# Optimization experiments

Hardware: AMD Instinct MI355X
Metric: run time of the kernel (lower is better)

## Reference

```python
import jax, jax.numpy as jnp
import numpy as np

B, N, D_PAIR, D_HID = 1, 512, 128, 128

def _layernorm(x, gamma, beta, eps=1e-5):
    mu = jnp.mean(x, axis=-1, keepdims=True)
    var = jnp.mean(jnp.square(x - mu), axis=-1, keepdims=True)
    return (x - mu) * jax.lax.rsqrt(var + eps) * gamma + beta

def setup_inputs() -> dict:
    key = jax.random.key(0)
    ks = jax.random.split(key, 8)
    s = 0.02  # small init scale for weights
    return {
        "z": jax.random.normal(ks[0], (B, N, N, D_PAIR), dtype=jnp.float32),
        "mask": jnp.ones((B, N, N), dtype=jnp.float32),
        "w_ab_p": jax.random.normal(ks[1], (2 * D_HID, D_PAIR), dtype=jnp.float32) * s,
        "b_ab_p": jnp.zeros((2 * D_HID,), dtype=jnp.float32),
        "w_ab_g": jax.random.normal(ks[2], (2 * D_HID, D_PAIR), dtype=jnp.float32) * s,
        "b_ab_g": jnp.zeros((2 * D_HID,), dtype=jnp.float32),
        "w_g": jax.random.normal(ks[3], (D_PAIR, D_PAIR), dtype=jnp.float32) * s,
        "b_g": jnp.zeros((D_PAIR,), dtype=jnp.float32),
        "w_z": jax.random.normal(ks[4], (D_PAIR, D_HID), dtype=jnp.float32) * s,
        "b_z": jnp.zeros((D_PAIR,), dtype=jnp.float32),
        "ln_in_g": jnp.ones((D_PAIR,), dtype=jnp.float32),
        "ln_in_b": jnp.zeros((D_PAIR,), dtype=jnp.float32),
        "ln_out_g": jnp.ones((D_HID,), dtype=jnp.float32),
        "ln_out_b": jnp.zeros((D_HID,), dtype=jnp.float32),
    }

def reference(z, mask, w_ab_p, b_ab_p, w_ab_g, b_ab_g, w_g, b_g, w_z, b_z,
              ln_in_g, ln_in_b, ln_out_g, ln_out_b):
    z_ = _layernorm(z, ln_in_g, ln_in_b)                      # [B,N,N,c_z]
    ab = (z_ @ w_ab_p.T + b_ab_p) * jax.nn.sigmoid(z_ @ w_ab_g.T + b_ab_g)
    ab = ab * mask[..., None]                                 # [B,N,N,2h]
    a, b = jnp.split(ab, 2, axis=-1)                          # [B,N,N,h] each
    # outgoing=True: sum over k of a[i,k,d]*b[j,k,d]
    x = jnp.einsum('bikd,bjkd->bijd', a, b)                   # [B,N,N,h]
    g = jax.nn.sigmoid(z @ w_g.T + b_g)                       # [B,N,N,c_z]
    out = g * (_layernorm(x, ln_out_g, ln_out_b) @ w_z.T + b_z)
    return out
```

## Files before the change

### kernel.cpp

```cpp
#include <hip/hip_runtime.h>
#include <stdint.h>

#define NSEQ 512
#define DPAIR 128
#define NN (NSEQ*NSEQ)
#define LDPAD 136

typedef unsigned short u16;
typedef __attribute__((ext_vector_type(8))) short bf16x8;
typedef __attribute__((ext_vector_type(4))) float f32x4;

__device__ __forceinline__ float bf2f(u16 h){ return __uint_as_float(((uint32_t)h)<<16); }
__device__ __forceinline__ u16 f2bf(float f){
  uint32_t u = __float_as_uint(f);
  u += 0x7fffu + ((u>>16)&1u);
  return (u16)(u>>16);
}
__device__ __forceinline__ uint32_t cvtpk(float lo, float hi){
  uint32_t r;
  asm("v_cvt_pk_bf16_f32 %0, %1, %2" : "=v"(r) : "v"(lo), "v"(hi));
  return r;
}
__device__ __forceinline__ float sigmoidf_(float x){ return 1.0f/(1.0f+__expf(-x)); }

__device__ __forceinline__ void stage_w64(const float* __restrict__ src, u16* wb, int t){
  const float4* ws = (const float4*)src;
  #pragma unroll
  for (int i=0;i<8;i++){
    int e4 = i*256 + t; int r = e4>>5, c4 = e4&31;
    float4 v = ws[e4];
    uint2 pk;
    pk.x = cvtpk(v.x, v.y);
    pk.y = cvtpk(v.z, v.w);
    *(uint2*)&wb[r*LDPAD + c4*4] = pk;
  }
}

__device__ __forceinline__ void gemm_64x64(const u16* A, const u16* W,
                                           int wm, int wn, int fr, int fq,
                                           f32x4 (&acc)[2][2]){
  #pragma unroll
  for (int kk=0;kk<4;kk++){
    bf16x8 aF[2], bF[2];
    #pragma unroll
    for (int mi=0;mi<2;mi++) aF[mi] = *(const bf16x8*)(A + (wm+mi*16+fr)*LDPAD + kk*32 + fq*8);
    #pragma unroll
    for (int ni=0;ni<2;ni++) bF[ni] = *(const bf16x8*)(W + (wn+ni*16+fr)*LDPAD + kk*32 + fq*8);
    #pragma unroll
    for (int mi=0;mi<2;mi++)
      #pragma unroll
      for (int ni=0;ni<2;ni++)
        acc[mi][ni] = __builtin_amdgcn_mfma_f32_16x16x32_bf16(aF[mi], bF[ni], acc[mi][ni], 0, 0, 0);
  }
}

__global__ __launch_bounds__(256) void k1_proj(
    const float* __restrict__ z, const float* __restrict__ mask,
    const float* __restrict__ w_ab_p, const float* __restrict__ b_ab_p,
    const float* __restrict__ w_ab_g, const float* __restrict__ b_ab_g,
    const float* __restrict__ w_g, const float* __restrict__ b_g,
    const float* __restrict__ ln_g, const float* __restrict__ ln_b,
    u16* __restrict__ a_t, u16* __restrict__ b_t, u16* __restrict__ g_out)
{
  __shared__ u16 zr[64*LDPAD];
  __shared__ u16 zn[64*LDPAD];
  __shared__ u16 wb[64*LDPAD];
  __shared__ float lng[DPAIR], lnb[DPAIR], msk[64];

  const int t = threadIdx.x;
  const int p0 = blockIdx.x * 64;
  const int lane = t & 63, wv = t >> 6;
  const int wm = (wv >> 1) * 32, wn = (wv & 1) * 32;
  const int fr = lane & 15, fq = lane >> 4;

  if (t < DPAIR){ lng[t] = ln_g[t]; lnb[t] = ln_b[t]; }
  else if (t < DPAIR + 64) msk[t - DPAIR] = mask[p0 + t - DPAIR];

  {
    const float4* zs = (const float4*)(z + (size_t)p0 * DPAIR);
    #pragma unroll
    for (int i=0;i<8;i++){
      int e4 = i*256 + t; int pos = e4>>5, c4 = e4&31;
      float4 v = zs[e4];
      uint2 pk;
      pk.x = cvtpk(v.x, v.y);
      pk.y = cvtpk(v.z, v.w);
      *(uint2*)&zr[pos*LDPAD + c4*4] = pk;
    }
  }
  __syncthreads();
  {
    int pos = t>>2, q = t&3;
    float s=0.f, s2=0.f;
    #pragma unroll
    for (int j=0;j<32;j++){ float v = bf2f(zr[pos*LDPAD + q*32 + j]); s += v; s2 += v*v; }
    s  += __shfl_xor(s, 1);  s2 += __shfl_xor(s2, 1);
    s  += __shfl_xor(s, 2);  s2 += __shfl_xor(s2, 2);
    float mu  = s * (1.f/128.f);
    float var = s2 * (1.f/128.f) - mu*mu;
    float rs  = rsqrtf(var + 1e-5f);
    #pragma unroll
    for (int j=0;j<32;j++){
      int c = q*32 + j;
      float v = bf2f(zr[pos*LDPAD + c]);
      zn[pos*LDPAD + c] = f2bf((v - mu)*rs*lng[c] + lnb[c]);
    }
  }

  for (int nt=0; nt<4; nt++){
    __syncthreads();
    stage_w64(w_ab_p + nt*64*DPAIR, wb, t);
    __syncthreads();
    f32x4 accP[2][2] = {};
    gemm_64x64(zn, wb, wm, wn, fr, fq, accP);
    __syncthreads();
    stage_w64(w_ab_g + nt*64*DPAIR, wb, t);
    __syncthreads();
    f32x4 accG[2][2] = {};
    gemm_64x64(zn, wb, wm, wn, fr, fq, accG);
    __syncthreads();
    #pragma unroll
    for (int mi=0;mi<2;mi++)
      #pragma unroll
      for (int ni=0;ni<2;ni++)
        #pragma unroll
        for (int r=0;r<4;r++){
          int pos = wm + mi*16 + fq*4 + r;
          int nl  = wn + ni*16 + fr;
          int ng  = nt*64 + nl;
          float p  = accP[mi][ni][r] + b_ab_p[ng];
          float gg = accG[mi][ni][r] + b_ab_g[ng];
          wb[nl*72 + pos] = f2bf(p * sigmoidf_(gg) * msk[pos]);
        }
    __syncthreads();
    u16* dst = (nt < 2) ? a_t : b_t;
    int dbase = (nt & 1) * 64;
    #pragma unroll
    for (int i=0;i<2;i++){
      int e8 = i*256 + t; int dl = e8>>3, pc = e8&7;
      uint4 v = *(const uint4*)&wb[dl*72 + pc*8];
      *(uint4*)&dst[(size_t)(dbase+dl)*NN + p0 + pc*8] = v;
    }
  }

  for (int nt=0; nt<2; nt++){
    __syncthreads();
    stage_w64(w_g + nt*64*DPAIR, wb, t);
    __syncthreads();
    f32x4 acc[2][2] = {};
    gemm_64x64(zr, wb, wm, wn, fr, fq, acc);
    #pragma unroll
    for (int mi=0;mi<2;mi++)
      #pragma unroll
      for (int ni=0;ni<2;ni++)
        #pragma unroll
        for (int r=0;r<4;r++){
          int pos = wm + mi*16 + fq*4 + r;
          int ng  = nt*64 + wn + ni*16 + fr;
          g_out[(size_t)(p0+pos)*DPAIR + ng] = f2bf(sigmoidf_(acc[mi][ni][r] + b_g[ng]));
        }
  }
}

__global__ __launch_bounds__(256) void k2_einsum(
    const u16* __restrict__ a_t, const u16* __restrict__ b_t, u16* __restrict__ x_t)
{
  __shared__ u16 As[128*40];
  __shared__ u16 Bs[128*40];
  const int t = threadIdx.x;
  const int d  = blockIdx.z;
  const int i0 = blockIdx.x * 128;
  const int j0 = blockIdx.y * 128;
  const u16* Ag = a_t + (size_t)d*NN + (size_t)i0*NSEQ;
  const u16* Bg = b_t + (size_t)d*NN + (size_t)j0*NSEQ;

  const int lane = t & 63, wv = t >> 6;
  const int wm = (wv >> 1) * 64, wn = (wv & 1) * 64;
  const int fr = lane & 15, fq = lane >> 4;

  f32x4 acc[4][4] = {};

  for (int k0 = 0; k0 < NSEQ; k0 += 32){
    __syncthreads();
    #pragma unroll
    for (int i=0;i<2;i++){
      int e = i*256 + t; int r = e>>2, c8 = e&3;
      uint4 va = *(const uint4*)(Ag + (size_t)r*NSEQ + k0 + c8*8);
      *(uint4*)&As[r*40 + c8*8] = va;
      uint4 vb = *(const uint4*)(Bg + (size_t)r*NSEQ + k0 + c8*8);
      *(uint4*)&Bs[r*40 + c8*8] = vb;
    }
    __syncthreads();
    bf16x8 aF[4], bF[4];
    #pragma unroll
    for (int mi=0;mi<4;mi++) aF[mi] = *(const bf16x8*)&As[(wm + mi*16 + fr)*40 + fq*8];
    #pragma unroll
    for (int ni=0;ni<4;ni++) bF[ni] = *(const bf16x8*)&Bs[(wn + ni*16 + fr)*40 + fq*8];
    #pragma unroll
    for (int mi=0;mi<4;mi++)
      #pragma unroll
      for (int ni=0;ni<4;ni++)
        acc[mi][ni] = __builtin_amdgcn_mfma_f32_16x16x32_bf16(aF[mi], bF[ni], acc[mi][ni], 0, 0, 0);
  }
  u16* Xg = x_t + (size_t)d*NN;
  #pragma unroll
  for (int mi=0;mi<4;mi++)
    #pragma unroll
    for (int ni=0;ni<4;ni++)
      #pragma unroll
      for (int r=0;r<4;r++){
        int row = i0 + wm + mi*16 + fq*4 + r;
        int col = j0 + wn + ni*16 + fr;
        Xg[(size_t)row*NSEQ + col] = f2bf(acc[mi][ni][r]);
      }
}

__global__ __launch_bounds__(256) void k3_out(
    const u16* __restrict__ x_t, const u16* __restrict__ g_in,
    const float* __restrict__ w_z, const float* __restrict__ b_z,
    const float* __restrict__ ln_g, const float* __restrict__ ln_b,
    float* __restrict__ out)
{
  __shared__ u16 xs[64*LDPAD];
  __shared__ u16 wz[DPAIR*LDPAD];
  __shared__ float lng[DPAIR], lnb[DPAIR], bzs[DPAIR];

  const int t = threadIdx.x;
  const int p0 = blockIdx.x * 64;
  if (t < DPAIR){ lng[t] = ln_g[t]; lnb[t] = ln_b[t]; bzs[t] = b_z[t]; }

  {
    const float4* ws = (const float4*)w_z;
    #pragma unroll
    for (int i=0;i<16;i++){
      int e4 = i*256 + t; int r = e4>>5, c4 = e4&31;
      float4 v = ws[e4];
      uint2 pk;
      pk.x = cvtpk(v.x, v.y);
      pk.y = cvtpk(v.z, v.w);
      *(uint2*)&wz[r*LDPAD + c4*4] = pk;
    }
  }
  {
    #pragma unroll
    for (int i=0;i<8;i++){
      int e = i*256 + t; int dd = e>>4, pc = e&15;
      uint2 v = *(const uint2*)(x_t + (size_t)dd*NN + p0 + pc*4);
      int pb = pc*4;
      xs[(pb+0)*LDPAD + dd] = (u16)(v.x & 0xffffu);
      xs[(pb+1)*LDPAD + dd] = (u16)(v.x >> 16);
      xs[(pb+2)*LDPAD + dd] = (u16)(v.y & 0xffffu);
      xs[(pb+3)*LDPAD + dd] = (u16)(v.y >> 16);
    }
  }
  __syncthreads();
  {
    int pos = t>>2, q = t&3;
    float s=0.f, s2=0.f;
    #pragma unroll
    for (int j=0;j<32;j++){ float v = bf2f(xs[pos*LDPAD + q*32 + j]); s += v; s2 += v*v; }
    s  += __shfl_xor(s, 1);  s2 += __shfl_xor(s2, 1);
    s  += __shfl_xor(s, 2);  s2 += __shfl_xor(s2, 2);
    float mu  = s * (1.f/128.f);
    float var = s2 * (1.f/128.f) - mu*mu;
    float rs  = rsqrtf(var + 1e-5f);
    #pragma unroll
    for (int j=0;j<32;j++){
      int c = q*32 + j;
      float v = bf2f(xs[pos*LDPAD + c]);
      xs[pos*LDPAD + c] = f2bf((v - mu)*rs*lng[c] + lnb[c]);
    }
  }
  __syncthreads();
  const int lane = t & 63, wv = t >> 6;
  const int wm = (wv >> 1) * 32, wn = (wv & 1) * 64;
  const int fr = lane & 15, fq = lane >> 4;
  f32x4 acc[2][4] = {};
  #pragma unroll
  for (int kk=0;kk<4;kk++){
    bf16x8 aF[2], bF[4];
    #pragma unroll
    for (int mi=0;mi<2;mi++) aF[mi] = *(const bf16x8*)&xs[(wm+mi*16+fr)*LDPAD + kk*32 + fq*8];
    #pragma unroll
    for (int ni=0;ni<4;ni++) bF[ni] = *(const bf16x8*)&wz[(wn+ni*16+fr)*LDPAD + kk*32 + fq*8];
    #pragma unroll
    for (int mi=0;mi<2;mi++)
      #pragma unroll
      for (int ni=0;ni<4;ni++)
        acc[mi][ni] = __builtin_amdgcn_mfma_f32_16x16x32_bf16(aF[mi], bF[ni], acc[mi][ni], 0, 0, 0);
  }
  #pragma unroll
  for (int mi=0;mi<2;mi++)
    #pragma unroll
    for (int ni=0;ni<4;ni++)
      #pragma unroll
      for (int r=0;r<4;r++){
        int pos = wm + mi*16 + fq*4 + r;
        int c   = wn + ni*16 + fr;
        float gv = bf2f(g_in[(size_t)(p0+pos)*DPAIR + c]);
        out[(size_t)(p0+pos)*DPAIR + c] = gv * (acc[mi][ni][r] + bzs[c]);
      }
}

extern "C" void kernel_launch(void* const* d_in, const int* in_sizes, int n_in,
                              void* d_out, int out_size, void* d_ws, size_t ws_size,
                              hipStream_t stream)
{
  const float* z        = (const float*)d_in[0];
  const float* mask     = (const float*)d_in[1];
  const float* w_ab_p   = (const float*)d_in[2];
  const float* b_ab_p   = (const float*)d_in[3];
  const float* w_ab_g   = (const float*)d_in[4];
  const float* b_ab_g   = (const float*)d_in[5];
  const float* w_g      = (const float*)d_in[6];
  const float* b_g      = (const float*)d_in[7];
  const float* w_z      = (const float*)d_in[8];
  const float* b_z      = (const float*)d_in[9];
  const float* ln_in_g  = (const float*)d_in[10];
  const float* ln_in_b  = (const float*)d_in[11];
  const float* ln_out_g = (const float*)d_in[12];
  const float* ln_out_b = (const float*)d_in[13];
  float* out = (float*)d_out;

  const size_t plane = (size_t)DPAIR * NN;
  if (ws_size < 4 * plane * sizeof(u16)) return;

  u16* a_t = (u16*)d_ws;
  u16* b_t = a_t + plane;
  u16* g_b = b_t + plane;
  u16* x_t = g_b + plane;

  k1_proj<<<dim3(NN/64), dim3(256), 0, stream>>>(
      z, mask, w_ab_p, b_ab_p, w_ab_g, b_ab_g, w_g, b_g, ln_in_g, ln_in_b, a_t, b_t, g_b);
  k2_einsum<<<dim3(4, 4, DPAIR), dim3(256), 0, stream>>>(a_t, b_t, x_t);
  k3_out<<<dim3(NN/64), dim3(256), 0, stream>>>(x_t, g_b, w_z, b_z, ln_out_g, ln_out_b, out);
}
```

Measured before the change: 568.9 us.

## Restructure projection kernel: fused P/G staging, in-place layernorm, direct stores

The projection kernel now computes the output gate GEMM first with the full 128-row w_g staged at once, then layernorms z in place, freeing the separate normalized buffer. Each of the four ab tiles stages the P and G weight halves together into a doubled buffer and runs both GEMMs in one loop, cutting barriers per tile from six to about one. Transposed a/b results go straight from registers to global memory as 4-element packed stores instead of through a shared-memory transpose. The cost is narrower global stores (8 bytes each, spread across strided rows) in place of 16-byte coalesced ones, and a different shared-memory footprint.

```diff
diff --git a/kernel.cpp b/kernel.cpp
--- a/kernel.cpp
+++ b/kernel.cpp
@@ -22,37 +22,6 @@
   return r;
 }
 __device__ __forceinline__ float sigmoidf_(float x){ return 1.0f/(1.0f+__expf(-x)); }
-
-__device__ __forceinline__ void stage_w64(const float* __restrict__ src, u16* wb, int t){
-  const float4* ws = (const float4*)src;
-  #pragma unroll
-  for (int i=0;i<8;i++){
-    int e4 = i*256 + t; int r = e4>>5, c4 = e4&31;
-    float4 v = ws[e4];
-    uint2 pk;
-    pk.x = cvtpk(v.x, v.y);
-    pk.y = cvtpk(v.z, v.w);
-    *(uint2*)&wb[r*LDPAD + c4*4] = pk;
-  }
-}
-
-__device__ __forceinline__ void gemm_64x64(const u16* A, const u16* W,
-                                           int wm, int wn, int fr, int fq,
-                                           f32x4 (&acc)[2][2]){
-  #pragma unroll
-  for (int kk=0;kk<4;kk++){
-    bf16x8 aF[2], bF[2];
-    #pragma unroll
-    for (int mi=0;mi<2;mi++) aF[mi] = *(const bf16x8*)(A + (wm+mi*16+fr)*LDPAD + kk*32 + fq*8);
-    #pragma unroll
-    for (int ni=0;ni<2;ni++) bF[ni] = *(const bf16x8*)(W + (wn+ni*16+fr)*LDPAD + kk*32 + fq*8);
-    #pragma unroll
-    for (int mi=0;mi<2;mi++)
-      #pragma unroll
-      for (int ni=0;ni<2;ni++)
-        acc[mi][ni] = __builtin_amdgcn_mfma_f32_16x16x32_bf16(aF[mi], bF[ni], acc[mi][ni], 0, 0, 0);
-  }
-}
 
 __global__ __launch_bounds__(256) void k1_proj(
     const float* __restrict__ z, const float* __restrict__ mask,
@@ -63,14 +32,12 @@
     u16* __restrict__ a_t, u16* __restrict__ b_t, u16* __restrict__ g_out)
 {
   __shared__ u16 zr[64*LDPAD];
-  __shared__ u16 zn[64*LDPAD];
-  __shared__ u16 wb[64*LDPAD];
+  __shared__ u16 wb[128*LDPAD];
   __shared__ float lng[DPAIR], lnb[DPAIR], msk[64];
 
   const int t = threadIdx.x;
   const int p0 = blockIdx.x * 64;
   const int lane = t & 63, wv = t >> 6;
-  const int wm = (wv >> 1) * 32, wn = (wv & 1) * 32;
   const int fr = lane & 15, fq = lane >> 4;
 
   if (t < DPAIR){ lng[t] = ln_g[t]; lnb[t] = ln_b[t]; }
@@ -88,7 +55,51 @@
       *(uint2*)&zr[pos*LDPAD + c4*4] = pk;
     }
   }
-  __syncthreads();
+  {
+    const float4* ws = (const float4*)w_g;
+    #pragma unroll
+    for (int i=0;i<16;i++){
+      int e4 = i*256 + t; int r = e4>>5, c4 = e4&31;
+      float4 v = ws[e4];
+      uint2 pk;
+      pk.x = cvtpk(v.x, v.y);
+      pk.y = cvtpk(v.z, v.w);
+      *(uint2*)&wb[r*LDPAD + c4*4] = pk;
+    }
+  }
+  __syncthreads();
+
+  {
+    const int wm = (wv>>1)*32, wn2 = (wv&1)*64;
+    f32x4 acc[2][4] = {};
+    #pragma unroll
+    for (int kk=0;kk<4;kk++){
+      bf16x8 aF[2], bF[4];
+      #pragma unroll
+      for (int mi=0;mi<2;mi++) aF[mi] = *(const bf16x8*)&zr[(wm+mi*16+fr)*LDPAD + kk*32 + fq*8];
+      #pragma unroll
+      for (int ni=0;ni<4;ni++) bF[ni] = *(const bf16x8*)&wb[(wn2+ni*16+fr)*LDPAD + kk*32 + fq*8];
+      #pragma unroll
+      for (int mi=0;mi<2;mi++)
+        #pragma unroll
+        for (int ni=0;ni<4;ni++)
+          acc[mi][ni] = __builtin_amdgcn_mfma_f32_16x16x32_bf16(aF[mi], bF[ni], acc[mi][ni], 0, 0, 0);
+    }
+    #pragma unroll
+    for (int mi=0;mi<2;mi++)
+      #pragma unroll
+      for (int ni=0;ni<4;ni++){
+        int ng = wn2 + ni*16 + fr;
+        float bg = b_g[ng];
+        #pragma unroll
+        for (int r=0;r<4;r++){
+          int pos = wm + mi*16 + fq*4 + r;
+          g_out[(size_t)(p0+pos)*DPAIR + ng] = f2bf(sigmoidf_(acc[mi][ni][r] + bg));
+        }
+      }
+  }
+  __syncthreads();
+
   {
     int pos = t>>2, q = t&3;
     float s=0.f, s2=0.f;
@@ -103,62 +114,78 @@
     for (int j=0;j<32;j++){
       int c = q*32 + j;
       float v = bf2f(zr[pos*LDPAD + c]);
-      zn[pos*LDPAD + c] = f2bf((v - mu)*rs*lng[c] + lnb[c]);
-    }
-  }
-
+      zr[pos*LDPAD + c] = f2bf((v - mu)*rs*lng[c] + lnb[c]);
+    }
+  }
+  __syncthreads();
+
+  const int wm = (wv >> 1) * 32, wn = (wv & 1) * 32;
   for (int nt=0; nt<4; nt++){
+    {
+      const float4* wsP = (const float4*)(w_ab_p + (size_t)nt*64*DPAIR);
+      const float4* wsG = (const float4*)(w_ab_g + (size_t)nt*64*DPAIR);
+      #pragma unroll
+      for (int i=0;i<8;i++){
+        int e4 = i*256 + t; int r = e4>>5, c4 = e4&31;
+        float4 v = wsP[e4];
+        uint2 pk;
+        pk.x = cvtpk(v.x, v.y);
+        pk.y = cvtpk(v.z, v.w);
+        *(uint2*)&wb[r*LDPAD + c4*4] = pk;
+      }
+      #pragma unroll
+      for (int i=0;i<8;i++){
+        int e4 = i*256 + t; int r = e4>>5, c4 = e4&31;
+        float4 v = wsG[e4];
+        uint2 pk;
+        pk.x = cvtpk(v.x, v.y);
+        pk.y = cvtpk(v.z, v.w);
+        *(uint2*)&wb[(64+r)*LDPAD + c4*4] = pk;
+      }
+    }
     __syncthreads();
-    stage_w64(w_ab_p + nt*64*DPAIR, wb, t);
-    __syncthreads();
-    f32x4 accP[2][2] = {};
-    gemm_64x64(zn, wb, wm, wn, fr, fq, accP);
-    __syncthreads();
-    stage_w64(w_ab_g + nt*64*DPAIR, wb, t);
-    __syncthreads();
-    f32x4 accG[2][2] = {};
-    gemm_64x64(zn, wb, wm, wn, fr, fq, accG);
-    __syncthreads();
-    #pragma unroll
-    for (int mi=0;mi<2;mi++)
-      #pragma unroll
-      for (int ni=0;ni<2;ni++)
+    f32x4 accP[2][2] = {}, accG[2][2] = {};
+    #pragma unroll
+    for (int kk=0;kk<4;kk++){
+      bf16x8 aF[2], bP[2], bG[2];
+      #pragma unroll
+      for (int mi=0;mi<2;mi++) aF[mi] = *(const bf16x8*)&zr[(wm+mi*16+fr)*LDPAD + kk*32 + fq*8];
+      #pragma unroll
+      for (int ni=0;ni<2;ni++){
+        bP[ni] = *(const bf16x8*)&wb[(wn+ni*16+fr)*LDPAD + kk*32 + fq*8];
+        bG[ni] = *(const bf16x8*)&wb[(64+wn+ni*16+fr)*LDPAD + kk*32 + fq*8];
+      }
+      #pragma unroll
+      for (int mi=0;mi<2;mi++)
         #pragma unroll
-        for (int r=0;r<4;r++){
-          int pos = wm + mi*16 + fq*4 + r;
-          int nl  = wn + ni*16 + fr;
-          int ng  = nt*64 + nl;
-          float p  = accP[mi][ni][r] + b_ab_p[ng];
-          float gg = accG[mi][ni][r] + b_ab_g[ng];
-          wb[nl*72 + pos] = f2bf(p * sigmoidf_(gg) * msk[pos]);
+        for (int ni=0;ni<2;ni++){
+          accP[mi][ni] = __builtin_amdgcn_mfma_f32_16x16x32_bf16(aF[mi], bP[ni], accP[mi][ni], 0, 0, 0);
+          accG[mi][ni] = __builtin_amdgcn_mfma_f32_16x16x32_bf16(aF[mi], bG[ni], accG[mi][ni], 0, 0, 0);
         }
-    __syncthreads();
+    }
     u16* dst = (nt < 2) ? a_t : b_t;
     int dbase = (nt & 1) * 64;
     #pragma unroll
-    for (int i=0;i<2;i++){
-      int e8 = i*256 + t; int dl = e8>>3, pc = e8&7;
-      uint4 v = *(const uint4*)&wb[dl*72 + pc*8];
-      *(uint4*)&dst[(size_t)(dbase+dl)*NN + p0 + pc*8] = v;
-    }
-  }
-
-  for (int nt=0; nt<2; nt++){
+    for (int mi=0;mi<2;mi++){
+      int posb = wm + mi*16 + fq*4;
+      #pragma unroll
+      for (int ni=0;ni<2;ni++){
+        int nl   = wn + ni*16 + fr;
+        int ng   = nt*64 + nl;
+        int drow = dbase + nl;
+        float bp  = b_ab_p[ng];
+        float bgv = b_ab_g[ng];
+        float v0 = (accP[mi][ni][0]+bp) * sigmoidf_(accG[mi][ni][0]+bgv) * msk[posb+0];
+        float v1 = (accP[mi][ni][1]+bp) * sigmoidf_(accG[mi][ni][1]+bgv) * msk[posb+1];
+        float v2 = (accP[mi][ni][2]+bp) * sigmoidf_(accG[mi][ni][2]+bgv) * msk[posb+2];
+        float v3 = (accP[mi][ni][3]+bp) * sigmoidf_(accG[mi][ni][3]+bgv) * msk[posb+3];
+        uint2 pk;
+        pk.x = (uint32_t)f2bf(v0) | ((uint32_t)f2bf(v1)<<16);
+        pk.y = (uint32_t)f2bf(v2) | ((uint32_t)f2bf(v3)<<16);
+        *(uint2*)&dst[(size_t)drow*NN + p0 + posb] = pk;
+      }
+    }
     __syncthreads();
-    stage_w64(w_g + nt*64*DPAIR, wb, t);
-    __syncthreads();
-    f32x4 acc[2][2] = {};
-    gemm_64x64(zr, wb, wm, wn, fr, fq, acc);
-    #pragma unroll
-    for (int mi=0;mi<2;mi++)
-      #pragma unroll
-      for (int ni=0;ni<2;ni++)
-        #pragma unroll
-        for (int r=0;r<4;r++){
-          int pos = wm + mi*16 + fq*4 + r;
-          int ng  = nt*64 + wn + ni*16 + fr;
-          g_out[(size_t)(p0+pos)*DPAIR + ng] = f2bf(sigmoidf_(acc[mi][ni][r] + b_g[ng]));
-        }
   }
 }
 
```

After: 567.6 us. About the same (-0.2%).
